# Kernel optimization log

Measured on AMD Instinct MI355X. Metric: run time of the kernel, lower is better.

## Reference

```python
import jax, jax.numpy as jnp
import numpy as np

N_NODES = 100000
N_EDGES = 800000
IN_DIM = 128
HID = 128
EMB = 2 * HID  # 256, embedding_dim = hidden_dim * 2
N_CLS = 16


def _glorot(key, shape):
    fan_in, fan_out = shape
    lim = jnp.sqrt(6.0 / (fan_in + fan_out)).astype(jnp.float32)
    return jax.random.uniform(key, shape, jnp.float32, -lim, lim)


def setup_inputs() -> dict:
    key = jax.random.key(0)
    ks = jax.random.split(key, 12)
    x = jax.random.normal(ks[0], (N_NODES, IN_DIM), jnp.float32)
    edge_index = jax.random.randint(ks[1], (2, N_EDGES), 0, N_NODES, jnp.int64)
    return {
        "x": x,
        "edge_index": edge_index,
        # layer 1: GraphConv(IN_DIM -> HID)
        "W_rel1": _glorot(ks[2], (IN_DIM, HID)),
        "W_root1": _glorot(ks[3], (IN_DIM, HID)),
        "b1": jnp.zeros((HID,), jnp.float32),
        # layer 2: GraphConv(HID -> EMB)
        "W_rel2": _glorot(ks[4], (HID, EMB)),
        "W_root2": _glorot(ks[5], (HID, EMB)),
        "b2": jnp.zeros((EMB,), jnp.float32),
        # layer 3: GraphConv(EMB -> N_CLS)
        "W_rel3": _glorot(ks[6], (EMB, N_CLS)),
        "W_root3": _glorot(ks[7], (EMB, N_CLS)),
        "b3": jnp.zeros((N_CLS,), jnp.float32),
    }


def _graph_conv(x, src, dst, W_rel, W_root, b):
    # PyG GraphConv: out = lin_rel(sum_{j in N(i)} x_j) + lin_root(x_i)
    agg = jax.ops.segment_sum(x[src], dst, num_segments=N_NODES)  # [N, F_in]
    return agg @ W_rel + x @ W_root + b


def reference(x, edge_index, W_rel1, W_root1, b1, W_rel2, W_root2, b2,
              W_rel3, W_root3, b3):
    src, dst = edge_index[0], edge_index[1]
    h = jax.nn.relu(_graph_conv(x, src, dst, W_rel1, W_root1, b1))
    # dropout skipped: eval mode (training=False)
    h = jax.nn.relu(_graph_conv(h, src, dst, W_rel2, W_root2, b2))
    h = _graph_conv(h, src, dst, W_rel3, W_root3, b3)
    return jax.nn.log_softmax(h, axis=1)
```

## Files before the change

### kernel.cpp

```cpp
#include <hip/hip_runtime.h>

#define NN 100000
#define NE 800000
#define NPAD 100096
#define OCT 12544

typedef __attribute__((ext_vector_type(8))) __bf16 bf16x8;
typedef __attribute__((ext_vector_type(4))) float f32x4;

__device__ __forceinline__ uint f2bf(float f) {
  uint u = __float_as_uint(f);
  return (u + 0x7fffu + ((u >> 16) & 1u)) >> 16;
}
__device__ __forceinline__ float bflo(uint u) { return __uint_as_float(u << 16); }
__device__ __forceinline__ float bfhi(uint u) { return __uint_as_float(u & 0xffff0000u); }

__device__ __forceinline__ bf16x8 cvt8(float4 a, float4 b) {
  uint4 u;
  u.x = f2bf(a.x) | (f2bf(a.y) << 16);
  u.y = f2bf(a.z) | (f2bf(a.w) << 16);
  u.z = f2bf(b.x) | (f2bf(b.y) << 16);
  u.w = f2bf(b.z) | (f2bf(b.w) << 16);
  return *(bf16x8*)&u;
}


__device__ __forceinline__ bf16x8 ldfrag(const ushort* base, int row, int kb) {
  int off = (row << 8) + (kb ^ ((row & 15) << 4));
  return *(const bf16x8*)((const char*)base + off);
}

__global__ __launch_bounds__(512, 4) void k_fuse1(
    const float* __restrict__ x, ushort* __restrict__ Y1, ushort* __restrict__ Z1,
    const float* __restrict__ Wr1, const float* __restrict__ Wo1,
    const float* __restrict__ Wr2, const float* __restrict__ Wo2,
    const float* __restrict__ Wr3, const float* __restrict__ Wo3,
    ushort* __restrict__ wt, const int* __restrict__ dst, int* __restrict__ deg) {
  __shared__ ushort sW[128 * 128];
  int b = blockIdx.x;
  int tid = threadIdx.x;

  if (b >= 2352) {
    int idx = 32768 + (b - 2352) * 512 + tid;
    float v;
    if (idx < 98304) {
      const float* W;
      int base;
      if (idx < 65536) { W = Wr2; base = 32768; }
      else { W = Wo2; base = 65536; }
      int li = idx - base;
      int o = li >> 7, k = li & 127;
      k = (k & 7) * 16 + (k >> 3);
      v = W[(size_t)k * 256 + o];
    } else {
      int li = idx - 98304;
      int o = li >> 8, p = li & 255;
      int k = (p & 15) * 16 + (p >> 4);
      v = (o < 16) ? Wr3[(size_t)k * 16 + o] : Wo3[(size_t)k * 16 + (o - 16)];
    }
    wt[idx] = (ushort)f2bf(v);
    return;
  }
  if (b >= 784) {
    int hb = b - 784;
    int xcd = hb & 7, chunk = hb >> 3;
    int e0 = chunk * 4096 + tid;
#pragma unroll
    for (int i = 0; i < 8; ++i) {
      int e = e0 + i * 512;
      if (e < NE) {
        int d = dst[e];
        if (d / OCT == xcd) atomicAdd(&deg[d], 1);
      }
    }
    return;
  }

  int half = (b >> 3) & 1;
  int pr = (b >> 4) * 8 + (b & 7);
  if (pr >= NPAD / 256) return;
  int r0 = pr * 256;

  int lane = tid & 63, wid = tid >> 6;
  int cl = lane & 15, hi = lane >> 4;
  int arow0 = r0 + wid * 32 + cl;
  int arow1 = arow0 + 16;
  const float* px0 = x + (size_t)(arow0 < NN ? arow0 : NN - 1) * 128;
  const float* px1 = x + (size_t)(arow1 < NN ? arow1 : NN - 1) * 128;

  float4 F0[2][2], F1[2][2];
#pragma unroll
  for (int s = 0; s < 2; ++s) {
    F0[s][0] = *(const float4*)(px0 + s * 32 + hi * 8);
    F0[s][1] = *(const float4*)(px0 + s * 32 + hi * 8 + 4);
    F1[s][0] = *(const float4*)(px1 + s * 32 + hi * 8);
    F1[s][1] = *(const float4*)(px1 + s * 32 + hi * 8 + 4);
  }

  {
    const float* Wsrc = half ? Wo1 : Wr1;
    int o = tid & 127;
    int kp = tid >> 7;
#pragma unroll
    for (int it = 0; it < 16; ++it) {
      int k0 = (it * 4 + kp) * 2;
      float w0 = Wsrc[(size_t)k0 * 128 + o];
      float w1 = Wsrc[(size_t)(k0 + 1) * 128 + o];
      uint u = f2bf(w0) | (f2bf(w1) << 16);
      int byte = (o << 8) + ((((k0 >> 3) << 4) ^ ((o & 15) << 4))) + (k0 & 7) * 2;
      *(uint*)((char*)sW + byte) = u;
    }
  }
  __syncthreads();

  f32x4 zero = {0.f, 0.f, 0.f, 0.f};
  f32x4 acc0[8], acc1[8];
#pragma unroll
  for (int j = 0; j < 8; ++j) { acc0[j] = zero; acc1[j] = zero; }

#pragma unroll
  for (int ks = 0; ks < 4; ++ks) {
    const int p = ks & 1;
    bf16x8 A0 = cvt8(F0[p][0], F0[p][1]);
    bf16x8 A1 = cvt8(F1[p][0], F1[p][1]);
    int kb = ks * 64 + hi * 16;
#pragma unroll
    for (int j = 0; j < 8; ++j) {
      bf16x8 wf = ldfrag(sW, j * 16 + cl, kb);
      acc0[j] = __builtin_amdgcn_mfma_f32_16x16x32_bf16(A0, wf, acc0[j], 0, 0, 0);
      acc1[j] = __builtin_amdgcn_mfma_f32_16x16x32_bf16(A1, wf, acc1[j], 0, 0, 0);
    }
    if (ks < 2) {
      F0[p][0] = *(const float4*)(px0 + (ks + 2) * 32 + hi * 8);
      F0[p][1] = *(const float4*)(px0 + (ks + 2) * 32 + hi * 8 + 4);
      F1[p][0] = *(const float4*)(px1 + (ks + 2) * 32 + hi * 8);
      F1[p][1] = *(const float4*)(px1 + (ks + 2) * 32 + hi * 8 + 4);
    }
  }

  ushort* tgt = half ? Z1 : Y1;
#pragma unroll
  for (int i = 0; i < 2; ++i) {
#pragma unroll
    for (int reg = 0; reg < 4; ++reg) {
      int row = r0 + wid * 32 + i * 16 + hi * 4 + reg;
      if (row < NN) {
        float a[8];
#pragma unroll
        for (int j = 0; j < 8; ++j) a[j] = i ? acc1[j][reg] : acc0[j][reg];
        uint4 u;
        u.x = f2bf(a[0]) | (f2bf(a[1]) << 16);
        u.y = f2bf(a[2]) | (f2bf(a[3]) << 16);
        u.z = f2bf(a[4]) | (f2bf(a[5]) << 16);
        u.w = f2bf(a[6]) | (f2bf(a[7]) << 16);
        *(uint4*)(tgt + (size_t)row * 128 + cl * 8) = u;
      }
    }
  }
}

__global__ void k_scan_partial(const int* __restrict__ deg, int* __restrict__ bsum, int N) {
  __shared__ int s[256];
  int b = blockIdx.x, t = threadIdx.x;
  int base = b * 1024 + t * 4;
  int v = 0;
#pragma unroll
  for (int i = 0; i < 4; ++i) { int idx = base + i; if (idx < N) v += deg[idx]; }
  s[t] = v; __syncthreads();
  for (int o = 128; o > 0; o >>= 1) { if (t < o) s[t] += s[t + o]; __syncthreads(); }
  if (t == 0) bsum[b] = s[0];
}

__global__ void k_scan_bsums(const int* __restrict__ bsum, int* __restrict__ bpre,
                             int* __restrict__ offsets, int NB, int N) {
  __shared__ int s[128];
  int t = threadIdx.x;
  int v = (t < NB) ? bsum[t] : 0;
  s[t] = v; __syncthreads();
  for (int o = 1; o < 128; o <<= 1) {
    int add = (t >= o) ? s[t - o] : 0;
    __syncthreads();
    s[t] += add;
    __syncthreads();
  }
  if (t < NB) bpre[t] = s[t] - v;
  if (t == NB - 1) offsets[N] = s[t];
}

__global__ void k_scan_final(const int* __restrict__ deg, const int* __restrict__ bpre,
                             int* __restrict__ offsets, int* __restrict__ cursor, int N) {
  __shared__ int s[256];
  int b = blockIdx.x, t = threadIdx.x;
  int base = b * 1024 + t * 4;
  int v[4];
#pragma unroll
  for (int i = 0; i < 4; ++i) { int idx = base + i; v[i] = (idx < N) ? deg[idx] : 0; }
  int tsum = v[0] + v[1] + v[2] + v[3];
  s[t] = tsum; __syncthreads();
  for (int o = 1; o < 256; o <<= 1) {
    int add = (t >= o) ? s[t - o] : 0;
    __syncthreads();
    s[t] += add;
    __syncthreads();
  }
  int run = s[t] - tsum + bpre[b];
#pragma unroll
  for (int i = 0; i < 4; ++i) {
    int idx = base + i;
    if (idx < N) { offsets[idx] = run; cursor[idx] = run; }
    run += v[i];
  }
}

__global__ __launch_bounds__(256) void k_scatter(const int* __restrict__ src,
                                                 const int* __restrict__ dst,
                                                 int* __restrict__ cursor,
                                                 int* __restrict__ csr_src) {
  int xcd = blockIdx.x & 7, chunk = blockIdx.x >> 3;
  int e0 = chunk * 2048 + threadIdx.x;
#pragma unroll
  for (int i = 0; i < 8; ++i) {
    int e = e0 + i * 256;
    if (e < NE) {
      int d = dst[e];
      if (d / OCT == xcd) {
        int pos = atomicAdd(&cursor[d], 1);
        csr_src[pos] = src[e];
      }
    }
  }
}

#define ACC8(q)                      \
  do {                               \
    acc[0] += bflo(q.x); acc[1] += bfhi(q.x); \
    acc[2] += bflo(q.y); acc[3] += bfhi(q.y); \
    acc[4] += bflo(q.z); acc[5] += bfhi(q.z); \
    acc[6] += bflo(q.w); acc[7] += bfhi(q.w); \
  } while (0)

__global__ __launch_bounds__(256) void k_agg_relu(const ushort* __restrict__ Y1,
                                                  const ushort* __restrict__ Z1,
                                                  const int* __restrict__ offsets,
                                                  const int* __restrict__ csr,
                                                  const float* __restrict__ bias,
                                                  ushort* __restrict__ h1) {
  int tid = threadIdx.x;
  int sg = tid >> 4, fl = tid & 15;
  int n = blockIdx.x * 16 + sg;
  if (n >= NN) return;
  int o0 = offsets[n], o1 = offsets[n + 1];
  const uint4* X4 = (const uint4*)Y1;
  float acc[8];
#pragma unroll
  for (int k = 0; k < 8; ++k) acc[k] = 0.f;
  int j = o0;
  if (j + 3 < o1) {
    uint4 q0 = X4[(size_t)csr[j] * 16 + fl];
    uint4 q1 = X4[(size_t)csr[j + 1] * 16 + fl];
    uint4 q2 = X4[(size_t)csr[j + 2] * 16 + fl];
    uint4 q3 = X4[(size_t)csr[j + 3] * 16 + fl];
    j += 4;
    while (j + 3 < o1) {
      uint4 p0 = X4[(size_t)csr[j] * 16 + fl];
      uint4 p1 = X4[(size_t)csr[j + 1] * 16 + fl];
      uint4 p2 = X4[(size_t)csr[j + 2] * 16 + fl];
      uint4 p3 = X4[(size_t)csr[j + 3] * 16 + fl];
      j += 4;
      ACC8(q0); ACC8(q1); ACC8(q2); ACC8(q3);
      q0 = p0; q1 = p1; q2 = p2; q3 = p3;
    }
    ACC8(q0); ACC8(q1); ACC8(q2); ACC8(q3);
  }
  for (; j < o1; ++j) {
    uint4 q = X4[(size_t)csr[j] * 16 + fl];
    ACC8(q);
  }
  uint4 zown = ((const uint4*)Z1)[(size_t)n * 16 + fl];
  float z[8] = {bflo(zown.x), bfhi(zown.x), bflo(zown.y), bfhi(zown.y),
                bflo(zown.z), bfhi(zown.z), bflo(zown.w), bfhi(zown.w)};
  float r[8];
#pragma unroll
  for (int jj = 0; jj < 8; ++jj) {
    r[jj] = fmaxf(acc[jj] + z[jj] + bias[jj * 16 + fl], 0.f);
  }
  uint4 o;
  o.x = f2bf(r[0]) | (f2bf(r[1]) << 16);
  o.y = f2bf(r[2]) | (f2bf(r[3]) << 16);
  o.z = f2bf(r[4]) | (f2bf(r[5]) << 16);
  o.w = f2bf(r[6]) | (f2bf(r[7]) << 16);
  ((uint4*)h1)[(size_t)n * 16 + fl] = o;
}

__global__ __launch_bounds__(256) void k_aggbf(const ushort* __restrict__ X,
                                               const int* __restrict__ offsets,
                                               const int* __restrict__ csr,
                                               ushort* __restrict__ out) {
  int tid = threadIdx.x;
  int sg = tid >> 4, fl = tid & 15;
  int n = blockIdx.x * 16 + sg;
  if (n >= NN) return;
  int o0 = offsets[n], o1 = offsets[n + 1];
  const uint4* X4 = (const uint4*)X;
  float acc[8];
#pragma unroll
  for (int k = 0; k < 8; ++k) acc[k] = 0.f;
  int j = o0;
  if (j + 3 < o1) {
    uint4 q0 = X4[(size_t)csr[j] * 16 + fl];
    uint4 q1 = X4[(size_t)csr[j + 1] * 16 + fl];
    uint4 q2 = X4[(size_t)csr[j + 2] * 16 + fl];
    uint4 q3 = X4[(size_t)csr[j + 3] * 16 + fl];
    j += 4;
    while (j + 3 < o1) {
      uint4 p0 = X4[(size_t)csr[j] * 16 + fl];
      uint4 p1 = X4[(size_t)csr[j + 1] * 16 + fl];
      uint4 p2 = X4[(size_t)csr[j + 2] * 16 + fl];
      uint4 p3 = X4[(size_t)csr[j + 3] * 16 + fl];
      j += 4;
      ACC8(q0); ACC8(q1); ACC8(q2); ACC8(q3);
      q0 = p0; q1 = p1; q2 = p2; q3 = p3;
    }
    ACC8(q0); ACC8(q1); ACC8(q2); ACC8(q3);
  }
  for (; j < o1; ++j) {
    uint4 q = X4[(size_t)csr[j] * 16 + fl];
    ACC8(q);
  }
  uint4 o;
  o.x = f2bf(acc[0]) | (f2bf(acc[1]) << 16);
  o.y = f2bf(acc[2]) | (f2bf(acc[3]) << 16);
  o.z = f2bf(acc[4]) | (f2bf(acc[5]) << 16);
  o.w = f2bf(acc[6]) | (f2bf(acc[7]) << 16);
  ((uint4*)out)[(size_t)n * 16 + fl] = o;
}

__global__ __launch_bounds__(512, 4) void k_gemm2l3(
    const ushort* __restrict__ Aagg, const ushort* __restrict__ Aroot,
    const ushort* __restrict__ Wrelt, const ushort* __restrict__ Wroott,
    const float* __restrict__ bias2, const ushort* __restrict__ Wt3,
    const float* __restrict__ bias3, ushort* __restrict__ y3b, float* __restrict__ z) {
  __shared__ ushort sW[256 * 128];
  int tid = threadIdx.x;
  int r0 = blockIdx.x * 128;
  int lane = tid & 63, wid = tid >> 6;
  int cl = lane & 15, hi = lane >> 4;
  int arow = r0 + wid * 16 + cl;
  const ushort* pa = Aagg + (size_t)arow * 128 + hi * 8;
  const ushort* pr = Aroot + (size_t)arow * 128 + hi * 8;

  bf16x8 Aa[2], Ar[2];
  Aa[0] = *(const bf16x8*)(pa);
  Aa[1] = *(const bf16x8*)(pa + 32);
  Ar[0] = *(const bf16x8*)(pr);
  Ar[1] = *(const bf16x8*)(pr + 32);

  {
    const char* gw = (const char*)Wrelt;
#pragma unroll
    for (int i = 0; i < 8; ++i) {
      int L = (tid + i * 512) << 4;
      int row = L >> 8;
      int gb = L ^ ((row & 15) << 4);
      __builtin_amdgcn_global_load_lds((const __attribute__((address_space(1))) void*)(gw + gb),
                                       (__attribute__((address_space(3))) void*)((char*)sW + L), 16, 0, 0);
    }
  }
  __syncthreads();

  f32x4 zero = {0.f, 0.f, 0.f, 0.f};
  f32x4 acc[16];
#pragma unroll
  for (int j = 0; j < 16; ++j) acc[j] = zero;

#pragma unroll
  for (int ks = 0; ks < 4; ++ks) {
    const int p = ks & 1;
    int kb = ks * 64 + hi * 16;
#pragma unroll
    for (int j = 0; j < 16; ++j) {
      bf16x8 wf = ldfrag(sW, j * 16 + cl, kb);
      acc[j] = __builtin_amdgcn_mfma_f32_16x16x32_bf16(Aa[p], wf, acc[j], 0, 0, 0);
    }
    if (ks < 2) Aa[p] = *(const bf16x8*)(pa + (ks + 2) * 32);
  }
  __syncthreads();

  {
    const char* gw = (const char*)Wroott;
#pragma unroll
    for (int i = 0; i < 8; ++i) {
      int L = (tid + i * 512) << 4;
      int row = L >> 8;
      int gb = L ^ ((row & 15) << 4);
      __builtin_amdgcn_global_load_lds((const __attribute__((address_space(1))) void*)(gw + gb),
                                       (__attribute__((address_space(3))) void*)((char*)sW + L), 16, 0, 0);
    }
  }
  __syncthreads();

#pragma unroll
  for (int ks = 0; ks < 4; ++ks) {
    const int p = ks & 1;
    int kb = ks * 64 + hi * 16;
#pragma unroll
    for (int j = 0; j < 16; ++j) {
      bf16x8 wf = ldfrag(sW, j * 16 + cl, kb);
      acc[j] = __builtin_amdgcn_mfma_f32_16x16x32_bf16(Ar[p], wf, acc[j], 0, 0, 0);
    }
    if (ks < 2) Ar[p] = *(const bf16x8*)(pr + (ks + 2) * 32);
  }
  __syncthreads();

  {
    float bv[16];
#pragma unroll
    for (int j = 0; j < 16; ++j) bv[j] = bias2[j * 16 + cl];
#pragma unroll
    for (int reg = 0; reg < 4; ++reg) {
      int rr = hi * 4 + reg;
      float v[16];
#pragma unroll
      for (int j = 0; j < 16; ++j) v[j] = fmaxf(acc[j][reg] + bv[j], 0.f);
      uint4 a, bq;
      a.x = f2bf(v[0]) | (f2bf(v[1]) << 16);
      a.y = f2bf(v[2]) | (f2bf(v[3]) << 16);
      a.z = f2bf(v[4]) | (f2bf(v[5]) << 16);
      a.w = f2bf(v[6]) | (f2bf(v[7]) << 16);
      bq.x = f2bf(v[8]) | (f2bf(v[9]) << 16);
      bq.y = f2bf(v[10]) | (f2bf(v[11]) << 16);
      bq.z = f2bf(v[12]) | (f2bf(v[13]) << 16);
      bq.w = f2bf(v[14]) | (f2bf(v[15]) << 16);
      int rowb = (wid * 16 + rr) * 512;
      *(uint4*)((char*)sW + rowb + ((cl * 32 + 0) ^ (rr << 4))) = a;
      *(uint4*)((char*)sW + rowb + ((cl * 32 + 16) ^ (rr << 4))) = bq;
    }
  }
  __syncthreads();

  f32x4 ay = zero, az = zero;
  const ushort* w3a = Wt3 + cl * 256 + hi * 8;
  const ushort* w3b = Wt3 + (16 + cl) * 256 + hi * 8;
#pragma unroll
  for (int ks = 0; ks < 8; ++ks) {
    int c = ks * 4 + hi;
    bf16x8 a = *(const bf16x8*)((const char*)sW + (wid * 16 + cl) * 512 + ((c * 16) ^ (cl << 4)));
    bf16x8 b0 = *(const bf16x8*)(w3a + ks * 32);
    bf16x8 b1 = *(const bf16x8*)(w3b + ks * 32);
    ay = __builtin_amdgcn_mfma_f32_16x16x32_bf16(a, b0, ay, 0, 0, 0);
    az = __builtin_amdgcn_mfma_f32_16x16x32_bf16(a, b1, az, 0, 0, 0);
  }
  float bv3 = bias3[cl];
#pragma unroll
  for (int reg = 0; reg < 4; ++reg) {
    int row = r0 + wid * 16 + hi * 4 + reg;
    if (row < NN) {
      y3b[(size_t)row * 16 + cl] = (ushort)f2bf(ay[reg]);
      z[(size_t)row * 16 + cl] = az[reg] + bv3;
    }
  }
}

__global__ void k_agg16lsm(const int* __restrict__ offsets, const int* __restrict__ csr,
                           const ushort* __restrict__ y3b, float* __restrict__ out) {
  int t = blockIdx.x * 256 + threadIdx.x;
  if (t >= NN * 8) return;
  int n = t >> 3, g = t & 7;
  int o0 = offsets[n], o1 = offsets[n + 1];
  float a0 = 0.f, a1 = 0.f;
  const uint* Y = (const uint*)y3b;
  for (int j = o0; j < o1; ++j) {
    uint u = Y[(size_t)csr[j] * 8 + g];
    a0 += bflo(u); a1 += bfhi(u);
  }
  float v0 = out[n * 16 + g * 2] + a0;
  float v1 = out[n * 16 + g * 2 + 1] + a1;
  float m = fmaxf(v0, v1);
#pragma unroll
  for (int mask = 1; mask < 8; mask <<= 1) m = fmaxf(m, __shfl_xor(m, mask));
  float s = __expf(v0 - m) + __expf(v1 - m);
#pragma unroll
  for (int mask = 1; mask < 8; mask <<= 1) s += __shfl_xor(s, mask);
  float ls = __logf(s);
  out[n * 16 + g * 2] = v0 - m - ls;
  out[n * 16 + g * 2 + 1] = v1 - m - ls;
}

extern "C" void kernel_launch(void* const* d_in, const int* in_sizes, int n_in,
                              void* d_out, int out_size, void* d_ws, size_t ws_size,
                              hipStream_t stream) {
  const float* x = (const float*)d_in[0];
  const int* ei = (const int*)d_in[1];
  const float* Wrel1 = (const float*)d_in[2];
  const float* Wroot1 = (const float*)d_in[3];
  const float* b1 = (const float*)d_in[4];
  const float* Wrel2 = (const float*)d_in[5];
  const float* Wroot2 = (const float*)d_in[6];
  const float* b2 = (const float*)d_in[7];
  const float* Wrel3 = (const float*)d_in[8];
  const float* Wroot3 = (const float*)d_in[9];
  const float* b3 = (const float*)d_in[10];
  float* out = (float*)d_out;

  char* ws = (char*)d_ws;
  size_t off = 0;
  auto alloc = [&](size_t bytes) {
    void* p = ws + off;
    off += (bytes + 255) / 256 * 256;
    return p;
  };
  int* deg = (int*)alloc((size_t)NN * 4);
  int* offsets = (int*)alloc((size_t)(NN + 1) * 4);
  int* cursor = (int*)alloc((size_t)NN * 4);
  int* bsum = (int*)alloc(128 * 4);
  int* bpre = (int*)alloc(128 * 4);
  int* csr = (int*)alloc((size_t)NE * 4);
  ushort* Y1 = (ushort*)alloc((size_t)NN * 128 * 2);
  ushort* Z1 = (ushort*)alloc((size_t)NN * 128 * 2);
  ushort* aggb = (ushort*)alloc((size_t)NPAD * 128 * 2);
  ushort* h1b = (ushort*)alloc((size_t)NPAD * 128 * 2);
  ushort* y3b = (ushort*)alloc((size_t)NN * 16 * 2);
  ushort* wt = (ushort*)alloc((size_t)106496 * 2);
  ushort *Wr2t = wt + 32768, *Wo2t = wt + 65536;
  ushort* Wt3 = wt + 98304;

  const int* src = ei;
  const int* dst = ei + NE;

  hipMemsetAsync(deg, 0, (size_t)NN * 4, stream);
  k_fuse1<<<2496, 512, 0, stream>>>(x, Y1, Z1, Wrel1, Wroot1, Wrel2, Wroot2, Wrel3,
                                    Wroot3, wt, dst, deg);

  int NB = (NN + 1023) / 1024;
  k_scan_partial<<<NB, 256, 0, stream>>>(deg, bsum, NN);
  k_scan_bsums<<<1, 128, 0, stream>>>(bsum, bpre, offsets, NB, NN);
  k_scan_final<<<NB, 256, 0, stream>>>(deg, bpre, offsets, cursor, NN);
  int nchunk = (NE + 2047) / 2048;
  k_scatter<<<8 * nchunk, 256, 0, stream>>>(src, dst, cursor, csr);

  k_agg_relu<<<NN / 16, 256, 0, stream>>>(Y1, Z1, offsets, csr, b1, h1b);
  k_aggbf<<<(NN + 15) / 16, 256, 0, stream>>>(h1b, offsets, csr, aggb);
  k_gemm2l3<<<NPAD / 128, 512, 0, stream>>>(aggb, h1b, Wr2t, Wo2t, b2, Wt3, b3, y3b, out);
  k_agg16lsm<<<(NN * 8 + 255) / 256, 256, 0, stream>>>(offsets, csr, y3b, out);
}
```

Before: 230.2 us.

## Fuse layer-2 neighbor aggregation into the GEMM kernel via LDS staging

Removes the separate aggregation kernel for layer 2. Each GEMM block now gathers neighbor rows of h1 for its 128 rows, sums them in registers, writes bf16 results into a swizzled LDS tile, and reads them back as MFMA A fragments. This drops the global write and re-read of the aggregated buffer and one kernel launch. The cost is that the irregular gather now runs inside a 512-thread GEMM kernel whose occupancy is bounded by its large LDS and register use, so latency hiding for the gather may be worse.

```diff
diff --git a/kernel.cpp b/kernel.cpp
--- a/kernel.cpp
+++ b/kernel.cpp
@@ -292,51 +292,9 @@
   ((uint4*)h1)[(size_t)n * 16 + fl] = o;
 }
 
-__global__ __launch_bounds__(256) void k_aggbf(const ushort* __restrict__ X,
-                                               const int* __restrict__ offsets,
-                                               const int* __restrict__ csr,
-                                               ushort* __restrict__ out) {
-  int tid = threadIdx.x;
-  int sg = tid >> 4, fl = tid & 15;
-  int n = blockIdx.x * 16 + sg;
-  if (n >= NN) return;
-  int o0 = offsets[n], o1 = offsets[n + 1];
-  const uint4* X4 = (const uint4*)X;
-  float acc[8];
-#pragma unroll
-  for (int k = 0; k < 8; ++k) acc[k] = 0.f;
-  int j = o0;
-  if (j + 3 < o1) {
-    uint4 q0 = X4[(size_t)csr[j] * 16 + fl];
-    uint4 q1 = X4[(size_t)csr[j + 1] * 16 + fl];
-    uint4 q2 = X4[(size_t)csr[j + 2] * 16 + fl];
-    uint4 q3 = X4[(size_t)csr[j + 3] * 16 + fl];
-    j += 4;
-    while (j + 3 < o1) {
-      uint4 p0 = X4[(size_t)csr[j] * 16 + fl];
-      uint4 p1 = X4[(size_t)csr[j + 1] * 16 + fl];
-      uint4 p2 = X4[(size_t)csr[j + 2] * 16 + fl];
-      uint4 p3 = X4[(size_t)csr[j + 3] * 16 + fl];
-      j += 4;
-      ACC8(q0); ACC8(q1); ACC8(q2); ACC8(q3);
-      q0 = p0; q1 = p1; q2 = p2; q3 = p3;
-    }
-    ACC8(q0); ACC8(q1); ACC8(q2); ACC8(q3);
-  }
-  for (; j < o1; ++j) {
-    uint4 q = X4[(size_t)csr[j] * 16 + fl];
-    ACC8(q);
-  }
-  uint4 o;
-  o.x = f2bf(acc[0]) | (f2bf(acc[1]) << 16);
-  o.y = f2bf(acc[2]) | (f2bf(acc[3]) << 16);
-  o.z = f2bf(acc[4]) | (f2bf(acc[5]) << 16);
-  o.w = f2bf(acc[6]) | (f2bf(acc[7]) << 16);
-  ((uint4*)out)[(size_t)n * 16 + fl] = o;
-}
-
 __global__ __launch_bounds__(512, 4) void k_gemm2l3(
-    const ushort* __restrict__ Aagg, const ushort* __restrict__ Aroot,
+    const ushort* __restrict__ h1, const int* __restrict__ offsets,
+    const int* __restrict__ csr,
     const ushort* __restrict__ Wrelt, const ushort* __restrict__ Wroott,
     const float* __restrict__ bias2, const ushort* __restrict__ Wt3,
     const float* __restrict__ bias3, ushort* __restrict__ y3b, float* __restrict__ z) {
@@ -345,15 +303,64 @@
   int r0 = blockIdx.x * 128;
   int lane = tid & 63, wid = tid >> 6;
   int cl = lane & 15, hi = lane >> 4;
+
   int arow = r0 + wid * 16 + cl;
-  const ushort* pa = Aagg + (size_t)arow * 128 + hi * 8;
-  const ushort* pr = Aroot + (size_t)arow * 128 + hi * 8;
-
-  bf16x8 Aa[2], Ar[2];
-  Aa[0] = *(const bf16x8*)(pa);
-  Aa[1] = *(const bf16x8*)(pa + 32);
-  Ar[0] = *(const bf16x8*)(pr);
-  Ar[1] = *(const bf16x8*)(pr + 32);
+  const ushort* prr = h1 + (size_t)arow * 128 + hi * 8;
+  bf16x8 Ar[4];
+#pragma unroll
+  for (int ks = 0; ks < 4; ++ks) Ar[ks] = *(const bf16x8*)(prr + ks * 32);
+
+  {
+    const uint4* X4 = (const uint4*)h1;
+#pragma unroll
+    for (int rr = 0; rr < 4; ++rr) {
+      int lr = wid * 16 + rr * 4 + hi;
+      int n = r0 + lr;
+      float acc[8];
+#pragma unroll
+      for (int k = 0; k < 8; ++k) acc[k] = 0.f;
+      if (n < NN) {
+        int o0 = offsets[n], o1 = offsets[n + 1];
+        int j = o0;
+        if (j + 3 < o1) {
+          uint4 q0 = X4[(size_t)csr[j] * 16 + cl];
+          uint4 q1 = X4[(size_t)csr[j + 1] * 16 + cl];
+          uint4 q2 = X4[(size_t)csr[j + 2] * 16 + cl];
+          uint4 q3 = X4[(size_t)csr[j + 3] * 16 + cl];
+          j += 4;
+          while (j + 3 < o1) {
+            uint4 p0 = X4[(size_t)csr[j] * 16 + cl];
+            uint4 p1 = X4[(size_t)csr[j + 1] * 16 + cl];
+            uint4 p2 = X4[(size_t)csr[j + 2] * 16 + cl];
+            uint4 p3 = X4[(size_t)csr[j + 3] * 16 + cl];
+            j += 4;
+            ACC8(q0); ACC8(q1); ACC8(q2); ACC8(q3);
+            q0 = p0; q1 = p1; q2 = p2; q3 = p3;
+          }
+          ACC8(q0); ACC8(q1); ACC8(q2); ACC8(q3);
+        }
+        for (; j < o1; ++j) {
+          uint4 q = X4[(size_t)csr[j] * 16 + cl];
+          ACC8(q);
+        }
+      }
+      uint4 o;
+      o.x = f2bf(acc[0]) | (f2bf(acc[1]) << 16);
+      o.y = f2bf(acc[2]) | (f2bf(acc[3]) << 16);
+      o.z = f2bf(acc[4]) | (f2bf(acc[5]) << 16);
+      o.w = f2bf(acc[6]) | (f2bf(acc[7]) << 16);
+      *(uint4*)((char*)sW + lr * 256 + ((cl * 16) ^ ((lr & 15) << 4))) = o;
+    }
+  }
+  __syncthreads();
+
+  bf16x8 Aa[4];
+#pragma unroll
+  for (int ks = 0; ks < 4; ++ks) {
+    int lr = wid * 16 + cl;
+    Aa[ks] = *(const bf16x8*)((const char*)sW + lr * 256 + (((ks * 64 + hi * 16)) ^ ((lr & 15) << 4)));
+  }
+  __syncthreads();
 
   {
     const char* gw = (const char*)Wrelt;
@@ -375,14 +382,12 @@
 
 #pragma unroll
   for (int ks = 0; ks < 4; ++ks) {
-    const int p = ks & 1;
     int kb = ks * 64 + hi * 16;
 #pragma unroll
     for (int j = 0; j < 16; ++j) {
       bf16x8 wf = ldfrag(sW, j * 16 + cl, kb);
-      acc[j] = __builtin_amdgcn_mfma_f32_16x16x32_bf16(Aa[p], wf, acc[j], 0, 0, 0);
-    }
-    if (ks < 2) Aa[p] = *(const bf16x8*)(pa + (ks + 2) * 32);
+      acc[j] = __builtin_amdgcn_mfma_f32_16x16x32_bf16(Aa[ks], wf, acc[j], 0, 0, 0);
+    }
   }
   __syncthreads();
 
@@ -401,14 +406,12 @@
 
 #pragma unroll
   for (int ks = 0; ks < 4; ++ks) {
-    const int p = ks & 1;
     int kb = ks * 64 + hi * 16;
 #pragma unroll
     for (int j = 0; j < 16; ++j) {
       bf16x8 wf = ldfrag(sW, j * 16 + cl, kb);
-      acc[j] = __builtin_amdgcn_mfma_f32_16x16x32_bf16(Ar[p], wf, acc[j], 0, 0, 0);
-    }
-    if (ks < 2) Ar[p] = *(const bf16x8*)(pr + (ks + 2) * 32);
+      acc[j] = __builtin_amdgcn_mfma_f32_16x16x32_bf16(Ar[ks], wf, acc[j], 0, 0, 0);
+    }
   }
   __syncthreads();
 
@@ -517,7 +520,6 @@
   int* csr = (int*)alloc((size_t)NE * 4);
   ushort* Y1 = (ushort*)alloc((size_t)NN * 128 * 2);
   ushort* Z1 = (ushort*)alloc((size_t)NN * 128 * 2);
-  ushort* aggb = (ushort*)alloc((size_t)NPAD * 128 * 2);
   ushort* h1b = (ushort*)alloc((size_t)NPAD * 128 * 2);
   ushort* y3b = (ushort*)alloc((size_t)NN * 16 * 2);
   ushort* wt = (ushort*)alloc((size_t)106496 * 2);
@@ -539,7 +541,7 @@
   k_scatter<<<8 * nchunk, 256, 0, stream>>>(src, dst, cursor, csr);
 
   k_agg_relu<<<NN / 16, 256, 0, stream>>>(Y1, Z1, offsets, csr, b1, h1b);
-  k_aggbf<<<(NN + 15) / 16, 256, 0, stream>>>(h1b, offsets, csr, aggb);
-  k_gemm2l3<<<NPAD / 128, 512, 0, stream>>>(aggb, h1b, Wr2t, Wo2t, b2, Wt3, b3, y3b, out);
+  k_gemm2l3<<<NPAD / 128, 512, 0, stream>>>(h1b, offsets, csr, Wr2t, Wo2t, b2, Wt3, b3,
+                                            y3b, out);
   k_agg16lsm<<<(NN * 8 + 255) / 256, 256, 0, stream>>>(offsets, csr, y3b, out);
 }
```

After: 238.7 us. 3.7% more time.
